# Kernel optimization log

Hardware: AMD Instinct MI355X
Metric: run time of the kernel (lower is better)

The kernel has to match this reference:

```python
import jax, jax.numpy as jnp
import numpy as np
import math

B, H, W = 8, 256, 256
CIN, COUT, K = 64, 64, 3
STYLE_IN = 512  # latent dim fed into EqualLinear
LIN_SCALE = 1.0 / math.sqrt(STYLE_IN)        # EqualLinear scale (lr_mul=1)
CONV_SCALE = 1.0 / math.sqrt(CIN * K * K)    # ModulatedConv2D scale


def setup_inputs() -> dict:
    key = jax.random.key(0)
    k1, k2, k3, k4 = jax.random.split(key, 4)
    inputs = jax.random.normal(k1, (B, H, W, CIN), dtype=jnp.float32)
    style = jax.random.normal(k2, (B, STYLE_IN), dtype=jnp.float32)
    # EqualLinear params: weight ~ N(0,1), bias init = 1
    mod_weight = jax.random.normal(k3, (STYLE_IN, CIN), dtype=jnp.float32)
    mod_bias = jnp.ones((CIN,), dtype=jnp.float32)
    # Conv weight [1, out_channel, in_channel, k, k] ~ N(0,1)
    weight = jax.random.normal(k4, (1, COUT, CIN, K, K), dtype=jnp.float32)
    return {"inputs": inputs, "style": style, "mod_weight": mod_weight,
            "mod_bias": mod_bias, "weight": weight}


def _per_sample_conv(xb, wb):
    # xb: [H, W, Cin]; wb: [Cout, Cin, K, K]
    w_hwio = jnp.transpose(wb, (2, 3, 1, 0))  # [K, K, Cin, Cout]
    y = jax.lax.conv_general_dilated(
        xb[None], w_hwio, window_strides=(1, 1), padding="SAME",
        dimension_numbers=("NHWC", "HWIO", "NHWC"))
    return y[0]


def reference(inputs, style, mod_weight, mod_bias, weight):
    # EqualLinear modulation: s = style @ (W * scale) + bias  -> [B, Cin]
    s = style @ (mod_weight * LIN_SCALE) + mod_bias
    # Modulate: [B, Cout, Cin, K, K]
    w = CONV_SCALE * weight * s[:, None, :, None, None]
    # Demodulate over (Cin, K, K)
    demod = jax.lax.rsqrt(jnp.sum(jnp.square(w), axis=(2, 3, 4)) + 1e-8)
    w = w * demod[:, :, None, None, None]
    # Grouped conv (groups = batch) == per-sample conv, vmapped over batch
    out = jax.vmap(_per_sample_conv)(inputs, w)  # [B, H, W, Cout]
    return out
```

## Files before the change

kernel.cpp:

```cpp
#include <hip/hip_runtime.h>

#define BATCH 8
#define HH 256
#define WW 256
#define CI 64
#define CO 64
#define STYLE_IN 512

typedef __bf16 bf16x8 __attribute__((ext_vector_type(8)));
typedef float  f32x4  __attribute__((ext_vector_type(4)));
typedef unsigned short u16x8 __attribute__((ext_vector_type(8)));

static __device__ inline unsigned short f2bf(float f) {
    union { float f; unsigned int u; } a; a.f = f;
    unsigned int u = a.u;
    u += 0x7fffu + ((u >> 16) & 1u);
    return (unsigned short)(u >> 16);
}

static __device__ inline bf16x8 as_bf(u16x8 v) {
    union { u16x8 u; bf16x8 b; } c; c.u = v; return c.b;
}

static __device__ inline void lds_barrier() {
    __builtin_amdgcn_sched_barrier(0);
    asm volatile("s_waitcnt lgkmcnt(0)" ::: "memory");
    __builtin_amdgcn_sched_barrier(0);
    __builtin_amdgcn_s_barrier();
    __builtin_amdgcn_sched_barrier(0);
}

__global__ __launch_bounds__(256) void modulate_kernel(
    const float* __restrict__ style, const float* __restrict__ mod_weight,
    const float* __restrict__ mod_bias, const float* __restrict__ weight,
    unsigned short* __restrict__ wbf)
{
    const int b   = blockIdx.x;
    const int oct = blockIdx.y;
    const int t   = threadIdx.x;
    __shared__ float sp[4][64];
    __shared__ float s_mod[64];
    __shared__ float dpart[8][32];
    __shared__ float demod[8];

    const float LIN_SCALE  = 0.044194173824159216f;
    const float CONV_SCALE = 0.041666666666666664f;

    {
        const int ci = t & 63, part = t >> 6;
        float acc = 0.f;
        const float* st = style + b * STYLE_IN + part * 128;
        const float* mw = mod_weight + part * 128 * 64 + ci;
        #pragma unroll 8
        for (int j = 0; j < 128; ++j) acc += st[j] * mw[j * 64];
        sp[part][ci] = acc;
    }
    __syncthreads();
    if (t < 64)
        s_mod[t] = (sp[0][t] + sp[1][t] + sp[2][t] + sp[3][t]) * LIN_SCALE + mod_bias[t];
    __syncthreads();

    {
        const int col = t >> 5, part = t & 31;
        float acc = 0.f;
        const float* wp = weight + (oct * 8 + col) * 576 + part * 18;
        #pragma unroll
        for (int ci2 = 0; ci2 < 2; ++ci2) {
            float s = s_mod[part * 2 + ci2];
            #pragma unroll
            for (int tp = 0; tp < 9; ++tp) {
                float v = wp[ci2 * 9 + tp] * s;
                acc += v * v;
            }
        }
        dpart[col][part] = acc * (CONV_SCALE * CONV_SCALE);
    }
    __syncthreads();
    if (t < 8) {
        float s = 0.f;
        #pragma unroll
        for (int p = 0; p < 32; ++p) s += dpart[t][p];
        demod[t] = rsqrtf(s + 1e-8f);
    }
    __syncthreads();

    for (int i = t; i < 4608; i += 256) {
        int ci  = i & 63;
        int col = (i >> 6) & 7;
        int tap = i >> 9;
        float v = CONV_SCALE * weight[(oct * 8 + col) * 576 + ci * 9 + tap]
                * s_mod[ci] * demod[col];
        wbf[((b * 9 + tap) * 64 + oct * 8 + col) * 64 + ci] = f2bf(v);
    }
}

#define PXS 72
#define ROWPX 130
#define ROW_ELEMS (ROWPX * PXS)

__global__ __launch_bounds__(256, 2) void conv_kernel(
    const float* __restrict__ x, const unsigned short* __restrict__ wbf,
    float* __restrict__ out)
{
    __shared__ unsigned short xs[4 * ROW_ELEMS];

    const int tid = threadIdx.x;
    const int x0  = blockIdx.x * 128;
    const int y0  = blockIdx.y * 8;
    const int b   = blockIdx.z;

    auto issue = [&](int yin, f32x4* v) {
        const bool rok = (unsigned)yin < (unsigned)HH;
        const float* src = x + ((size_t)(b * HH + (rok ? yin : 0))) * WW * CI;
        #pragma unroll
        for (int k = 0; k < 5; ++k) {
            int i  = tid + k * 256;
            int px = i >> 3, cg = i & 7;
            int xin = x0 - 1 + px;
            bool ok = rok && ((unsigned)xin < (unsigned)WW) && (i < 1040);
            const float* p = src + (size_t)xin * CI + cg * 8;
            f32x4 z = {0.f, 0.f, 0.f, 0.f};
            v[2 * k]     = ok ? *(const f32x4*)p       : z;
            v[2 * k + 1] = ok ? *(const f32x4*)(p + 4) : z;
        }
    };
    auto commit = [&](int slot, const f32x4* v) {
        unsigned short* dst = xs + slot * ROW_ELEMS;
        #pragma unroll
        for (int k = 0; k < 5; ++k) {
            int i = tid + k * 256;
            if (k == 4 && i >= 1040) continue;
            int px = i >> 3, cg = i & 7;
            u16x8 u;
            #pragma unroll
            for (int e = 0; e < 4; ++e) {
                u[e]     = f2bf(v[2 * k][e]);
                u[e + 4] = f2bf(v[2 * k + 1][e]);
            }
            *(u16x8*)&dst[px * PXS + cg * 8] = u;
        }
    };

    {
        f32x4 v[10];
        issue(y0 - 1, v); commit(0, v);
        issue(y0,     v); commit(1, v);
        issue(y0 + 1, v); commit(2, v);
    }

    const int wave = tid >> 6, lane = tid & 63;
    const int lm = lane & 15, lq = lane >> 4;
    const int wr = wave >> 1;
    const int wc = wave & 1;
    const int p0 = wr * 64;

    u16x8 wreg[9][2][2];
    {
        const unsigned short* wl = wbf + (size_t)b * 9 * 4096
                                 + (size_t)(wc * 32 + lm) * 64 + lq * 8;
        #pragma unroll
        for (int tap = 0; tap < 9; ++tap)
            #pragma unroll
            for (int ni = 0; ni < 2; ++ni)
                #pragma unroll
                for (int ks = 0; ks < 2; ++ks)
                    wreg[tap][ni][ks] =
                        *(const u16x8*)(wl + tap * 4096 + ni * 1024 + ks * 32);
    }
    #pragma unroll
    for (int tap = 0; tap < 9; ++tap)
        #pragma unroll
        for (int ni = 0; ni < 2; ++ni)
            #pragma unroll
            for (int ks = 0; ks < 2; ++ks)
                asm volatile("" : "+v"(wreg[tap][ni][ks]));

    __syncthreads();

    const int aoff_lane = (p0 + lm) * PXS + lq * 8;

    f32x4 vbuf[10];
    issue(y0 + 2, vbuf);

    #pragma unroll
    for (int j = 0; j < 8; ++j) {
        const int y = y0 + j;

        f32x4 acc[4][2];
        #pragma unroll
        for (int mi = 0; mi < 4; ++mi)
            #pragma unroll
            for (int ni = 0; ni < 2; ++ni)
                acc[mi][ni] = (f32x4){0.f, 0.f, 0.f, 0.f};

        const unsigned short* bases[3] = {
            xs + ((y)     & 3) * ROW_ELEMS,
            xs + ((y + 1) & 3) * ROW_ELEMS,
            xs + ((y + 2) & 3) * ROW_ELEMS,
        };

        #pragma unroll
        for (int kh = 0; kh < 3; ++kh) {
            const unsigned short* bs = bases[kh] + aoff_lane;
            #pragma unroll
            for (int kw = 0; kw < 3; ++kw) {
                #pragma unroll
                for (int ks = 0; ks < 2; ++ks) {
                    #pragma unroll
                    for (int mi = 0; mi < 4; ++mi) {
                        bf16x8 xf = *(const bf16x8*)(bs + (mi * 16 + kw) * PXS + ks * 32);
                        acc[mi][0] = __builtin_amdgcn_mfma_f32_16x16x32_bf16(
                            as_bf(wreg[kh * 3 + kw][0][ks]), xf, acc[mi][0], 0, 0, 0);
                        acc[mi][1] = __builtin_amdgcn_mfma_f32_16x16x32_bf16(
                            as_bf(wreg[kh * 3 + kw][1][ks]), xf, acc[mi][1], 0, 0, 0);
                    }
                }
            }
        }

        float* op = out + ((size_t)(b * HH + y) * WW + x0) * CO;
        #pragma unroll
        for (int mi = 0; mi < 4; ++mi) {
            int pix = p0 + mi * 16 + lm;
            #pragma unroll
            for (int ni = 0; ni < 2; ++ni)
                __builtin_nontemporal_store(acc[mi][ni],
                    (f32x4*)(op + (size_t)pix * CO + wc * 32 + ni * 16 + lq * 4));
        }

        commit((y + 3) & 3, vbuf);

        lds_barrier();

        if (j < 7) issue(y + 3, vbuf);
    }
}

extern "C" void kernel_launch(void* const* d_in, const int* in_sizes, int n_in,
                              void* d_out, int out_size, void* d_ws, size_t ws_size,
                              hipStream_t stream) {
    const float* inputs     = (const float*)d_in[0];
    const float* style      = (const float*)d_in[1];
    const float* mod_weight = (const float*)d_in[2];
    const float* mod_bias   = (const float*)d_in[3];
    const float* weight     = (const float*)d_in[4];
    float* out = (float*)d_out;
    unsigned short* wbf = (unsigned short*)d_ws;

    modulate_kernel<<<dim3(BATCH, 8), 256, 0, stream>>>(style, mod_weight, mod_bias, weight, wbf);
    conv_kernel<<<dim3(2, 32, BATCH), 256, 0, stream>>>(inputs, wbf, out);
}
```

Before: 278.8 us.

## Shrink conv tile to 64 pixels and split output channels across waves

The conv block now covers 64 pixels instead of 128, and each wave owns 16 output channels across all 64 pixels rather than 32 channels across 64 pixels. This halves the weight registers and accumulators per wave, which lets launch bounds request 4 blocks per CU and doubles the grid. The next-row global load is now issued after the MFMA loop instead of being prefetched a full iteration ahead, so less load latency is hidden inside one block. In exchange, each LDS activation fragment now feeds only one MFMA instead of two, and the halo overhead per block grows.

```diff
diff --git a/kernel.cpp b/kernel.cpp
--- a/kernel.cpp
+++ b/kernel.cpp
@@ -94,18 +94,19 @@
     }
 }
 
+#define BPX 64
 #define PXS 72
-#define ROWPX 130
+#define ROWPX 66
 #define ROW_ELEMS (ROWPX * PXS)
 
-__global__ __launch_bounds__(256, 2) void conv_kernel(
+__global__ __launch_bounds__(256, 4) void conv_kernel(
     const float* __restrict__ x, const unsigned short* __restrict__ wbf,
     float* __restrict__ out)
 {
     __shared__ unsigned short xs[4 * ROW_ELEMS];
 
     const int tid = threadIdx.x;
-    const int x0  = blockIdx.x * 128;
+    const int x0  = blockIdx.x * BPX;
     const int y0  = blockIdx.y * 8;
     const int b   = blockIdx.z;
 
@@ -113,11 +114,11 @@
         const bool rok = (unsigned)yin < (unsigned)HH;
         const float* src = x + ((size_t)(b * HH + (rok ? yin : 0))) * WW * CI;
         #pragma unroll
-        for (int k = 0; k < 5; ++k) {
+        for (int k = 0; k < 3; ++k) {
             int i  = tid + k * 256;
             int px = i >> 3, cg = i & 7;
             int xin = x0 - 1 + px;
-            bool ok = rok && ((unsigned)xin < (unsigned)WW) && (i < 1040);
+            bool ok = rok && ((unsigned)xin < (unsigned)WW) && (i < 528);
             const float* p = src + (size_t)xin * CI + cg * 8;
             f32x4 z = {0.f, 0.f, 0.f, 0.f};
             v[2 * k]     = ok ? *(const f32x4*)p       : z;
@@ -127,9 +128,9 @@
     auto commit = [&](int slot, const f32x4* v) {
         unsigned short* dst = xs + slot * ROW_ELEMS;
         #pragma unroll
-        for (int k = 0; k < 5; ++k) {
+        for (int k = 0; k < 3; ++k) {
             int i = tid + k * 256;
-            if (k == 4 && i >= 1040) continue;
+            if (k == 2 && i >= 528) continue;
             int px = i >> 3, cg = i & 7;
             u16x8 u;
             #pragma unroll
@@ -142,7 +143,7 @@
     };
 
     {
-        f32x4 v[10];
+        f32x4 v[6];
         issue(y0 - 1, v); commit(0, v);
         issue(y0,     v); commit(1, v);
         issue(y0 + 1, v); commit(2, v);
@@ -150,48 +151,35 @@
 
     const int wave = tid >> 6, lane = tid & 63;
     const int lm = lane & 15, lq = lane >> 4;
-    const int wr = wave >> 1;
-    const int wc = wave & 1;
-    const int p0 = wr * 64;
-
-    u16x8 wreg[9][2][2];
+
+    u16x8 wreg[9][2];
     {
         const unsigned short* wl = wbf + (size_t)b * 9 * 4096
-                                 + (size_t)(wc * 32 + lm) * 64 + lq * 8;
+                                 + (size_t)(wave * 16 + lm) * 64 + lq * 8;
         #pragma unroll
         for (int tap = 0; tap < 9; ++tap)
             #pragma unroll
-            for (int ni = 0; ni < 2; ++ni)
-                #pragma unroll
-                for (int ks = 0; ks < 2; ++ks)
-                    wreg[tap][ni][ks] =
-                        *(const u16x8*)(wl + tap * 4096 + ni * 1024 + ks * 32);
+            for (int ks = 0; ks < 2; ++ks)
+                wreg[tap][ks] = *(const u16x8*)(wl + tap * 4096 + ks * 32);
     }
     #pragma unroll
     for (int tap = 0; tap < 9; ++tap)
         #pragma unroll
-        for (int ni = 0; ni < 2; ++ni)
-            #pragma unroll
-            for (int ks = 0; ks < 2; ++ks)
-                asm volatile("" : "+v"(wreg[tap][ni][ks]));
-
-    __syncthreads();
-
-    const int aoff_lane = (p0 + lm) * PXS + lq * 8;
-
-    f32x4 vbuf[10];
-    issue(y0 + 2, vbuf);
+        for (int ks = 0; ks < 2; ++ks)
+            asm volatile("" : "+v"(wreg[tap][ks]));
+
+    __syncthreads();
+
+    const int aoff_lane = lm * PXS + lq * 8;
 
     #pragma unroll
     for (int j = 0; j < 8; ++j) {
         const int y = y0 + j;
 
-        f32x4 acc[4][2];
+        f32x4 acc[4];
         #pragma unroll
         for (int mi = 0; mi < 4; ++mi)
-            #pragma unroll
-            for (int ni = 0; ni < 2; ++ni)
-                acc[mi][ni] = (f32x4){0.f, 0.f, 0.f, 0.f};
+            acc[mi] = (f32x4){0.f, 0.f, 0.f, 0.f};
 
         const unsigned short* bases[3] = {
             xs + ((y)     & 3) * ROW_ELEMS,
@@ -206,33 +194,33 @@
             for (int kw = 0; kw < 3; ++kw) {
                 #pragma unroll
                 for (int ks = 0; ks < 2; ++ks) {
+                    bf16x8 xf[4];
                     #pragma unroll
-                    for (int mi = 0; mi < 4; ++mi) {
-                        bf16x8 xf = *(const bf16x8*)(bs + (mi * 16 + kw) * PXS + ks * 32);
-                        acc[mi][0] = __builtin_amdgcn_mfma_f32_16x16x32_bf16(
-                            as_bf(wreg[kh * 3 + kw][0][ks]), xf, acc[mi][0], 0, 0, 0);
-                        acc[mi][1] = __builtin_amdgcn_mfma_f32_16x16x32_bf16(
-                            as_bf(wreg[kh * 3 + kw][1][ks]), xf, acc[mi][1], 0, 0, 0);
-                    }
+                    for (int mi = 0; mi < 4; ++mi)
+                        xf[mi] = *(const bf16x8*)(bs + (mi * 16 + kw) * PXS + ks * 32);
+                    #pragma unroll
+                    for (int mi = 0; mi < 4; ++mi)
+                        acc[mi] = __builtin_amdgcn_mfma_f32_16x16x32_bf16(
+                            as_bf(wreg[kh * 3 + kw][ks]), xf[mi], acc[mi], 0, 0, 0);
                 }
             }
         }
 
+        f32x4 v[6];
+        if (j < 7) issue(y + 2, v);
+
         float* op = out + ((size_t)(b * HH + y) * WW + x0) * CO;
         #pragma unroll
         for (int mi = 0; mi < 4; ++mi) {
-            int pix = p0 + mi * 16 + lm;
-            #pragma unroll
-            for (int ni = 0; ni < 2; ++ni)
-                __builtin_nontemporal_store(acc[mi][ni],
-                    (f32x4*)(op + (size_t)pix * CO + wc * 32 + ni * 16 + lq * 4));
-        }
-
-        commit((y + 3) & 3, vbuf);
-
-        lds_barrier();
-
-        if (j < 7) issue(y + 3, vbuf);
+            int pix = mi * 16 + lm;
+            __builtin_nontemporal_store(acc[mi],
+                (f32x4*)(op + (size_t)pix * CO + wave * 16 + lq * 4));
+        }
+
+        if (j < 7) {
+            commit((y + 3) & 3, v);
+            lds_barrier();
+        }
     }
 }
 
@@ -248,5 +236,5 @@
     unsigned short* wbf = (unsigned short*)d_ws;
 
     modulate_kernel<<<dim3(BATCH, 8), 256, 0, stream>>>(style, mod_weight, mod_bias, weight, wbf);
-    conv_kernel<<<dim3(2, 32, BATCH), 256, 0, stream>>>(inputs, wbf, out);
-}
+    conv_kernel<<<dim3(WW / BPX, HH / 8, BATCH), 256, 0, stream>>>(inputs, wbf, out);
+}
```

Measured after the change: 294.1 us. 5.5% more time.
